# Optimization experiments

Measured on AMD Instinct MI355X. Metric: run time of the kernel, lower is better.

## Reference

```python
import jax, jax.numpy as jnp
import numpy as np

B, DZ, L = 1, 128, 256
H, DC = 4, 32
DHC = H * DC


def setup_inputs() -> dict:
    key = jax.random.key(0)
    ks = jax.random.split(key, 6)
    s = 0.02
    return {
        "z": jax.random.normal(ks[0], (B, DZ, L, L), dtype=jnp.float32),
        "ln_w": jnp.ones((DZ,), jnp.float32),
        "ln_b": jnp.zeros((DZ,), jnp.float32),
        "wq": jax.random.normal(ks[1], (DZ, DHC), jnp.float32) * s,
        "bq": jnp.zeros((DHC,), jnp.float32),
        "wk": jax.random.normal(ks[2], (DZ, DHC), jnp.float32) * s,
        "bk": jnp.zeros((DHC,), jnp.float32),
        "wv": jax.random.normal(ks[3], (DZ, DHC), jnp.float32) * s,
        "bv": jnp.zeros((DHC,), jnp.float32),
        "wg": jax.random.normal(ks[4], (DZ, DHC), jnp.float32) * s,
        "bg": jnp.zeros((DHC,), jnp.float32),
        "w2": jax.random.normal(ks[5], (DHC, DZ), jnp.float32) * s,
        "b2": jnp.zeros((DZ,), jnp.float32),
    }


def reference(z, ln_w, ln_b, wq, bq, wk, bk, wv, bv, wg, bg, w2, b2):
    # z: (B, C, L, L) -> (B, n, i, dz)
    zp = jnp.transpose(z, (0, 2, 3, 1))
    # LayerNorm over last dim (torch eps=1e-5)
    mu = jnp.mean(zp, axis=-1, keepdims=True)
    var = jnp.mean(jnp.square(zp - mu), axis=-1, keepdims=True)
    zn = (zp - mu) * jax.lax.rsqrt(var + 1e-5) * ln_w + ln_b

    def proj(w, b):  # (B,n,i,dz) -> (B,n,i,H,DC)
        return (zn @ w + b).reshape(zn.shape[:-1] + (H, DC))

    scalar = jnp.sqrt(jnp.float32(1.0 / DC))
    q = proj(wq, bq)
    k = proj(wk, bk)
    v = proj(wv, bv)
    attn = jnp.einsum('bnihc,bnjhc->bhnij', q * scalar, k)
    attn_w = jax.nn.softmax(attn, axis=-1)
    o = jnp.einsum('bhnij,bnjhc->bnihc', attn_w, v)
    g = jax.nn.sigmoid(zn @ wg + bg).reshape(o.shape)
    zo = (o * g).reshape(o.shape[:-2] + (DHC,))
    out = (zo @ w2 + b2)
    return jnp.transpose(out, (0, 3, 1, 2))  # (B, C, L, L)
```

## Files before the change

kernel.cpp:

```cpp
#include <hip/hip_runtime.h>
#include <cstdint>
#include <cstddef>

#define DZc   128
#define Lc    256
#define Hc    4
#define DCc   32
#define DHCc  128
#define NPOSc (Lc * Lc)

typedef __attribute__((ext_vector_type(8))) short bf16x8;
typedef __attribute__((ext_vector_type(4))) short bf16x4;
typedef __attribute__((ext_vector_type(4))) float f32x4;

static __device__ __forceinline__ unsigned short f2bf(float f) {
  unsigned u = __float_as_uint(f);
  u += 0x7FFFu + ((u >> 16) & 1u);
  return (unsigned short)(u >> 16);
}
static __device__ __forceinline__ float bf2f(unsigned short h) {
  return __uint_as_float(((unsigned)h) << 16);
}
static __device__ __forceinline__ float sigmoidf_(float x) {
  return 1.0f / (1.0f + __expf(-x));
}
static __device__ __forceinline__ unsigned cvtpk(float lo, float hi) {
  unsigned r;
  asm("v_cvt_pk_bf16_f32 %0, %1, %2" : "=v"(r) : "v"(lo), "v"(hi));
  return r;
}

__global__ __launch_bounds__(256) void prep_weights(
    const float* __restrict__ wq, const float* __restrict__ wk,
    const float* __restrict__ wv, const float* __restrict__ wg,
    const float* __restrict__ w2, unsigned short* __restrict__ wT)
{
  const int b = blockIdx.x;
  const int t = threadIdx.x;
  const float* src = (b == 0) ? wq : (b == 1) ? wk : (b == 2) ? wv : (b == 3) ? wg : w2;
  unsigned short* dst = wT + (size_t)b * (DZc * DHCc);
  const float scale = (b == 0) ? 0.17677669529663687f : 1.0f;
  for (int p = 0; p < 64; ++p) {
    const int idx = p * 256 + t;
    const int kk = idx >> 7, j = idx & 127;
    dst[j * 128 + kk] = f2bf(src[idx] * scale);
  }
}

__global__ __launch_bounds__(512, 2) void fused_ln_proj_attn(
    const float* __restrict__ z, const float* __restrict__ lnw, const float* __restrict__ lnb,
    const unsigned short* __restrict__ wT,
    const float* __restrict__ bq, const float* __restrict__ bk,
    const float* __restrict__ bv, const float* __restrict__ bg,
    unsigned short* __restrict__ og_ws)
{
  __shared__ unsigned short zkl[Lc * DZc];
  __shared__ unsigned short vtl[DHCc * Lc];
  __shared__ unsigned short pll[8][16 * 64];

  const int t  = threadIdx.x;
  const int n  = blockIdx.x;
  const int w8 = t >> 6;
  const int l  = t & 63;
  const int lr = l & 15;
  const int lg = l >> 4;
  const int h     = w8 & 3;
  const int ihalf = w8 >> 2;

  char* zkb = reinterpret_cast<char*>(zkl);
  char* vtb = reinterpret_cast<char*>(vtl);
  char* plb = reinterpret_cast<char*>(&pll[w8][0]);

  #pragma unroll
  for (int p = 0; p < 2; ++p) {
    const int pq = t >> 4;
    const int cg = t & 15;
    const int gp = n * 256 + p * 128 + pq * 4;
    const int cbase = cg * 8;

    float4 zr[8];
    #pragma unroll
    for (int cc = 0; cc < 8; ++cc)
      zr[cc] = *reinterpret_cast<const float4*>(&z[(size_t)(cbase + cc) * NPOSc + gp]);

    float s[4] = {0.f, 0.f, 0.f, 0.f}, s2[4] = {0.f, 0.f, 0.f, 0.f};
    #pragma unroll
    for (int cc = 0; cc < 8; ++cc) {
      s[0] += zr[cc].x; s2[0] += zr[cc].x * zr[cc].x;
      s[1] += zr[cc].y; s2[1] += zr[cc].y * zr[cc].y;
      s[2] += zr[cc].z; s2[2] += zr[cc].z * zr[cc].z;
      s[3] += zr[cc].w; s2[3] += zr[cc].w * zr[cc].w;
    }
    #pragma unroll
    for (int m = 1; m <= 8; m <<= 1) {
      #pragma unroll
      for (int e = 0; e < 4; ++e) {
        s[e]  += __shfl_xor(s[e],  m);
        s2[e] += __shfl_xor(s2[e], m);
      }
    }
    float mu[4], rs[4];
    #pragma unroll
    for (int e = 0; e < 4; ++e) {
      mu[e] = s[e] * (1.0f / DZc);
      const float var = s2[e] * (1.0f / DZc) - mu[e] * mu[e];
      rs[e] = rsqrtf(var + 1e-5f);
    }
    float lw[8], lb[8];
    #pragma unroll
    for (int q4 = 0; q4 < 2; ++q4) {
      const float4 a = *reinterpret_cast<const float4*>(&lnw[cbase + q4 * 4]);
      const float4 b = *reinterpret_cast<const float4*>(&lnb[cbase + q4 * 4]);
      lw[q4 * 4 + 0] = a.x; lw[q4 * 4 + 1] = a.y; lw[q4 * 4 + 2] = a.z; lw[q4 * 4 + 3] = a.w;
      lb[q4 * 4 + 0] = b.x; lb[q4 * 4 + 1] = b.y; lb[q4 * 4 + 2] = b.z; lb[q4 * 4 + 3] = b.w;
    }
    #pragma unroll
    for (int e = 0; e < 4; ++e) {
      const int i = p * 128 + pq * 4 + e;
      float zn[8];
      #pragma unroll
      for (int cc = 0; cc < 8; ++cc) {
        const float zc = (e == 0) ? zr[cc].x : (e == 1) ? zr[cc].y
                       : (e == 2) ? zr[cc].z : zr[cc].w;
        zn[cc] = (zc - mu[e]) * rs[e] * lw[cc] + lb[cc];
      }
      uint4 pw;
      pw.x = cvtpk(zn[0], zn[1]); pw.y = cvtpk(zn[2], zn[3]);
      pw.z = cvtpk(zn[4], zn[5]); pw.w = cvtpk(zn[6], zn[7]);
      int byte = i * 256 + cbase * 2;
      byte ^= ((i & 15) << 4);
      *reinterpret_cast<uint4*>(zkb + byte) = pw;
    }
  }
  __syncthreads();

  const unsigned short* wqT = wT;
  const unsigned short* wkT = wT + 1 * (DZc * DHCc);
  const unsigned short* wvT = wT + 2 * (DZc * DHCc);
  const unsigned short* wgT = wT + 3 * (DZc * DHCc);

  bf16x8 qfrag[8];
  {
    bf16x8 bfq[2][4];
    float4 qb4[2];
    #pragma unroll
    for (int jt = 0; jt < 2; ++jt) {
      #pragma unroll
      for (int kt = 0; kt < 4; ++kt)
        bfq[jt][kt] = *reinterpret_cast<const bf16x8*>(
            &wqT[(size_t)(h * 32 + jt * 16 + lr) * 128 + kt * 32 + lg * 8]);
      qb4[jt] = *reinterpret_cast<const float4*>(&bq[h * 32 + jt * 16 + lg * 4]);
      qb4[jt].x *= 0.17677669529663687f; qb4[jt].y *= 0.17677669529663687f;
      qb4[jt].z *= 0.17677669529663687f; qb4[jt].w *= 0.17677669529663687f;
    }
    #pragma unroll
    for (int it = 0; it < 8; ++it) {
      bf16x8 af[4];
      #pragma unroll
      for (int kt = 0; kt < 4; ++kt) {
        const int i = ihalf * 128 + it * 16 + lr;
        int byte = i * 256 + (kt * 64 + lg * 16);
        byte ^= ((i & 15) << 4);
        af[kt] = *reinterpret_cast<const bf16x8*>(zkb + byte);
      }
      f32x4 qa[2];
      qa[0] = (f32x4){0.f, 0.f, 0.f, 0.f};
      qa[1] = (f32x4){0.f, 0.f, 0.f, 0.f};
      #pragma unroll
      for (int kt = 0; kt < 4; ++kt)
        #pragma unroll
        for (int jt = 0; jt < 2; ++jt)
          qa[jt] = __builtin_amdgcn_mfma_f32_16x16x32_bf16(bfq[jt][kt], af[kt], qa[jt], 0, 0, 0);
      unsigned srcw0[2], srcw1[2];
      srcw0[0] = cvtpk(qa[0][0] + qb4[0].x, qa[0][1] + qb4[0].y);
      srcw0[1] = cvtpk(qa[0][2] + qb4[0].z, qa[0][3] + qb4[0].w);
      srcw1[0] = cvtpk(qa[1][0] + qb4[1].x, qa[1][1] + qb4[1].y);
      srcw1[1] = cvtpk(qa[1][2] + qb4[1].z, qa[1][3] + qb4[1].w);
      unsigned qw[4];
      #pragma unroll
      for (int i4 = 0; i4 < 4; ++i4) {
        const int quad = lg * 2 + (i4 >> 1);
        const int srcl = (quad & 3) * 16 + lr;
        const unsigned a = (unsigned)__shfl((int)srcw0[i4 & 1], srcl);
        const unsigned b = (unsigned)__shfl((int)srcw1[i4 & 1], srcl);
        qw[i4] = (lg >= 2) ? b : a;
      }
      uint4 qv; qv.x = qw[0]; qv.y = qw[1]; qv.z = qw[2]; qv.w = qw[3];
      qfrag[it] = *reinterpret_cast<const bf16x8*>(&qv);
    }
  }

  unsigned gpk[8][2][2];
  {
    bf16x8 bfg[2][4];
    float gb[2];
    #pragma unroll
    for (int jt = 0; jt < 2; ++jt) {
      #pragma unroll
      for (int kt = 0; kt < 4; ++kt)
        bfg[jt][kt] = *reinterpret_cast<const bf16x8*>(
            &wgT[(size_t)(h * 32 + jt * 16 + lr) * 128 + kt * 32 + lg * 8]);
      gb[jt] = bg[h * 32 + jt * 16 + lr];
    }
    #pragma unroll
    for (int it = 0; it < 8; ++it) {
      bf16x8 af[4];
      #pragma unroll
      for (int kt = 0; kt < 4; ++kt) {
        const int i = ihalf * 128 + it * 16 + lr;
        int byte = i * 256 + (kt * 64 + lg * 16);
        byte ^= ((i & 15) << 4);
        af[kt] = *reinterpret_cast<const bf16x8*>(zkb + byte);
      }
      f32x4 ga[2];
      ga[0] = (f32x4){0.f, 0.f, 0.f, 0.f};
      ga[1] = (f32x4){0.f, 0.f, 0.f, 0.f};
      #pragma unroll
      for (int kt = 0; kt < 4; ++kt)
        #pragma unroll
        for (int jt = 0; jt < 2; ++jt)
          ga[jt] = __builtin_amdgcn_mfma_f32_16x16x32_bf16(af[kt], bfg[jt][kt], ga[jt], 0, 0, 0);
      #pragma unroll
      for (int jt = 0; jt < 2; ++jt) {
        gpk[it][jt][0] = cvtpk(sigmoidf_(ga[jt][0] + gb[jt]), sigmoidf_(ga[jt][1] + gb[jt]));
        gpk[it][jt][1] = cvtpk(sigmoidf_(ga[jt][2] + gb[jt]), sigmoidf_(ga[jt][3] + gb[jt]));
      }
    }
  }

  {
    const int chq = w8 & 3, vih = w8 >> 2;
    bf16x8 bfv[2][4];
    float vb[2];
    #pragma unroll
    for (int jt = 0; jt < 2; ++jt) {
      #pragma unroll
      for (int kt = 0; kt < 4; ++kt)
        bfv[jt][kt] = *reinterpret_cast<const bf16x8*>(
            &wvT[(size_t)(chq * 32 + jt * 16 + lr) * 128 + kt * 32 + lg * 8]);
      vb[jt] = bv[chq * 32 + jt * 16 + lr];
    }
    #pragma unroll 1
    for (int it = 0; it < 8; ++it) {
      bf16x8 af[4];
      #pragma unroll
      for (int kt = 0; kt < 4; ++kt) {
        const int i = vih * 128 + it * 16 + lr;
        int byte = i * 256 + (kt * 64 + lg * 16);
        byte ^= ((i & 15) << 4);
        af[kt] = *reinterpret_cast<const bf16x8*>(zkb + byte);
      }
      f32x4 va[2];
      va[0] = (f32x4){0.f, 0.f, 0.f, 0.f};
      va[1] = (f32x4){0.f, 0.f, 0.f, 0.f};
      #pragma unroll
      for (int kt = 0; kt < 4; ++kt)
        #pragma unroll
        for (int jt = 0; jt < 2; ++jt)
          va[jt] = __builtin_amdgcn_mfma_f32_16x16x32_bf16(af[kt], bfv[jt][kt], va[jt], 0, 0, 0);
      const int ii0 = vih * 128 + it * 16 + lg * 4;
      #pragma unroll
      for (int jt = 0; jt < 2; ++jt) {
        const int ch = chq * 32 + jt * 16 + lr;
        uint2 pv;
        pv.x = cvtpk(va[jt][0] + vb[jt], va[jt][1] + vb[jt]);
        pv.y = cvtpk(va[jt][2] + vb[jt], va[jt][3] + vb[jt]);
        int byte = ch * 512 + ii0 * 2;
        byte ^= ((ch & 7) << 4);
        *reinterpret_cast<uint2*>(vtb + byte) = pv;
      }
    }
  }

  {
    bf16x8 bfk[4];
    #pragma unroll
    for (int kt = 0; kt < 4; ++kt)
      bfk[kt] = *reinterpret_cast<const bf16x8*>(
          &wkT[(size_t)(w8 * 16 + lr) * 128 + kt * 32 + lg * 8]);
    const float4 kb4 = *reinterpret_cast<const float4*>(&bk[w8 * 16 + lg * 4]);
    const float kb[4] = {kb4.x, kb4.y, kb4.z, kb4.w};

    #pragma unroll 1
    for (int c = 0; c < 4; ++c) {
      bf16x8 afr[4][4];
      #pragma unroll
      for (int itc = 0; itc < 4; ++itc)
        #pragma unroll
        for (int kt = 0; kt < 4; ++kt) {
          const int i = c * 64 + itc * 16 + lr;
          int byte = i * 256 + (kt * 64 + lg * 16);
          byte ^= ((i & 15) << 4);
          afr[itc][kt] = *reinterpret_cast<const bf16x8*>(zkb + byte);
        }
      __syncthreads();
      #pragma unroll
      for (int itc = 0; itc < 4; ++itc) {
        f32x4 ka = (f32x4){0.f, 0.f, 0.f, 0.f};
        #pragma unroll
        for (int kt = 0; kt < 4; ++kt)
          ka = __builtin_amdgcn_mfma_f32_16x16x32_bf16(bfk[kt], afr[itc][kt], ka, 0, 0, 0);
        const int j = c * 64 + itc * 16 + lr;
        uint2 pkk;
        pkk.x = cvtpk(ka[0] + kb[0], ka[1] + kb[1]);
        pkk.y = cvtpk(ka[2] + kb[2], ka[3] + kb[3]);
        int byte = j * 256 + (w8 * 16 + lg * 4) * 2;
        byte ^= ((j & 15) << 4);
        *reinterpret_cast<uint2*>(zkb + byte) = pkk;
      }
      __syncthreads();
    }
  }

  #pragma unroll
  for (int it = 0; it < 8; ++it) {
    f32x4 sacc[16];
    #pragma unroll
    for (int jt = 0; jt < 16; ++jt) sacc[jt] = (f32x4){0.f, 0.f, 0.f, 0.f};
    #pragma unroll
    for (int jt = 0; jt < 16; ++jt) {
      const int j = jt * 16 + lr;
      int byte = j * 256 + h * 64 + lg * 16;
      byte ^= ((j & 15) << 4);
      bf16x8 kf = *reinterpret_cast<const bf16x8*>(zkb + byte);
      sacc[jt] = __builtin_amdgcn_mfma_f32_16x16x32_bf16(kf, qfrag[it], sacc[jt], 0, 0, 0);
    }

    float psum = 0.f;
    #pragma unroll
    for (int jt = 0; jt < 16; ++jt)
      #pragma unroll
      for (int r = 0; r < 4; ++r) {
        const float e = __expf(sacc[jt][r]);
        sacc[jt][r] = e;
        psum += e;
      }
    psum += __shfl_xor(psum, 16);
    psum += __shfl_xor(psum, 32);
    const float rl = 1.0f / psum;

    f32x4 oacc[2];
    oacc[0] = (f32x4){0.f, 0.f, 0.f, 0.f};
    oacc[1] = (f32x4){0.f, 0.f, 0.f, 0.f};
    #pragma unroll
    for (int qr = 0; qr < 4; ++qr) {
      #pragma unroll
      for (int jj = 0; jj < 4; ++jj) {
        const int jt = qr * 4 + jj;
        uint2 pk;
        pk.x = cvtpk(sacc[jt][0], sacc[jt][1]);
        pk.y = cvtpk(sacc[jt][2], sacc[jt][3]);
        int byte = lr * 128 + (jj * 16 + lg * 4) * 2;
        byte ^= ((lr & 7) << 4);
        *reinterpret_cast<uint2*>(plb + byte) = pk;
      }
      asm volatile("s_waitcnt lgkmcnt(0)" ::: "memory");
      __builtin_amdgcn_sched_barrier(0);
      #pragma unroll
      for (int kq = 0; kq < 2; ++kq) {
        int pbyte = lr * 128 + (kq * 64 + lg * 16);
        pbyte ^= ((lr & 7) << 4);
        bf16x8 pf = *reinterpret_cast<const bf16x8*>(plb + pbyte);
        #pragma unroll
        for (int cht = 0; cht < 2; ++cht) {
          const int ch = h * 32 + cht * 16 + lr;
          int vbyte = ch * 512 + (qr * 128 + kq * 64 + lg * 16);
          vbyte ^= ((ch & 7) << 4);
          bf16x8 vf = *reinterpret_cast<const bf16x8*>(vtb + vbyte);
          oacc[cht] = __builtin_amdgcn_mfma_f32_16x16x32_bf16(pf, vf, oacc[cht], 0, 0, 0);
        }
      }
    }

    #pragma unroll
    for (int cht = 0; cht < 2; ++cht)
      #pragma unroll
      for (int r = 0; r < 4; ++r) {
        const int i = ihalf * 128 + it * 16 + lg * 4 + r;
        const float gv = bf2f((unsigned short)((gpk[it][cht][r >> 1] >> ((r & 1) * 16)) & 0xffff));
        const size_t off = ((size_t)(n * Lc + i)) * 128 + h * 32 + cht * 16 + lr;
        og_ws[off] = f2bf(oacc[cht][r] * rl * gv);
      }
  }
}

__global__ __launch_bounds__(256) void outproj_mfma(
    const unsigned short* __restrict__ og_ws,
    const unsigned short* __restrict__ w2T, const float* __restrict__ b2,
    float* __restrict__ out)
{
  const int t = threadIdx.x;
  const int w = t >> 6, l = t & 63, lr = l & 15, lg = l >> 4;
  const int pos = blockIdx.x * 64 + w * 16 + lr;

  bf16x8 zb[4];
  #pragma unroll
  for (int kt = 0; kt < 4; ++kt)
    zb[kt] = *reinterpret_cast<const bf16x8*>(
        &og_ws[(size_t)pos * 128 + kt * 32 + lg * 8]);

  #pragma unroll
  for (int ct = 0; ct < 8; ++ct) {
    f32x4 acc = (f32x4){0.f, 0.f, 0.f, 0.f};
    #pragma unroll
    for (int kt = 0; kt < 4; ++kt) {
      bf16x8 af = *reinterpret_cast<const bf16x8*>(
          &w2T[(size_t)(ct * 16 + lr) * 128 + kt * 32 + lg * 8]);
      acc = __builtin_amdgcn_mfma_f32_16x16x32_bf16(af, zb[kt], acc, 0, 0, 0);
    }
    #pragma unroll
    for (int r = 0; r < 4; ++r) {
      const int c = ct * 16 + lg * 4 + r;
      out[(size_t)c * NPOSc + pos] = acc[r] + b2[c];
    }
  }
}

extern "C" void kernel_launch(void* const* d_in, const int* in_sizes, int n_in,
                              void* d_out, int out_size, void* d_ws, size_t ws_size,
                              hipStream_t stream) {
  const float* z   = (const float*)d_in[0];
  const float* lnw = (const float*)d_in[1];
  const float* lnb = (const float*)d_in[2];
  const float* wq  = (const float*)d_in[3];
  const float* bq  = (const float*)d_in[4];
  const float* wk  = (const float*)d_in[5];
  const float* bk  = (const float*)d_in[6];
  const float* wv  = (const float*)d_in[7];
  const float* bv  = (const float*)d_in[8];
  const float* wg  = (const float*)d_in[9];
  const float* bg  = (const float*)d_in[10];
  const float* w2  = (const float*)d_in[11];
  const float* b2  = (const float*)d_in[12];
  float* out = (float*)d_out;

  const size_t S = (size_t)NPOSc * DHCc;
  unsigned short* ws = (unsigned short*)d_ws;
  unsigned short* og_ws = ws;
  unsigned short* wT    = ws + S;

  prep_weights<<<5, 256, 0, stream>>>(wq, wk, wv, wg, w2, wT);
  fused_ln_proj_attn<<<Lc, 512, 0, stream>>>(
      z, lnw, lnb, wT, bq, bk, bv, bg, og_ws);
  outproj_mfma<<<NPOSc / 64, 256, 0, stream>>>(
      og_ws, wT + 4 * (DZc * DHCc), b2, out);
}
```

Before: 80.07 us.

## Use 1024-thread blocks with 16 waves splitting rows into quarters

Doubles the fused attention block from 8 to 16 wavefronts. Each wave now handles a quarter of the query rows per head instead of a half, and the LN, Q/G/V/K projection loops are re-split to match. The goal is more parallel waves per row-block, hiding latency and cutting per-wave serial work. In exchange, each CU holds one large block instead of two, shared memory grows for the extra P buffers, and the per-thread register budget tightens.

```diff
diff --git a/kernel.cpp b/kernel.cpp
--- a/kernel.cpp
+++ b/kernel.cpp
@@ -47,7 +47,7 @@
   }
 }
 
-__global__ __launch_bounds__(512, 2) void fused_ln_proj_attn(
+__global__ __launch_bounds__(1024) void fused_ln_proj_attn(
     const float* __restrict__ z, const float* __restrict__ lnw, const float* __restrict__ lnb,
     const unsigned short* __restrict__ wT,
     const float* __restrict__ bq, const float* __restrict__ bk,
@@ -56,26 +56,25 @@
 {
   __shared__ unsigned short zkl[Lc * DZc];
   __shared__ unsigned short vtl[DHCc * Lc];
-  __shared__ unsigned short pll[8][16 * 64];
+  __shared__ unsigned short pll[16][16 * 64];
 
   const int t  = threadIdx.x;
   const int n  = blockIdx.x;
-  const int w8 = t >> 6;
+  const int w16 = t >> 6;
   const int l  = t & 63;
   const int lr = l & 15;
   const int lg = l >> 4;
-  const int h     = w8 & 3;
-  const int ihalf = w8 >> 2;
+  const int h  = w16 & 3;
+  const int iq = w16 >> 2;
 
   char* zkb = reinterpret_cast<char*>(zkl);
   char* vtb = reinterpret_cast<char*>(vtl);
-  char* plb = reinterpret_cast<char*>(&pll[w8][0]);
-
-  #pragma unroll
-  for (int p = 0; p < 2; ++p) {
+  char* plb = reinterpret_cast<char*>(&pll[w16][0]);
+
+  {
     const int pq = t >> 4;
     const int cg = t & 15;
-    const int gp = n * 256 + p * 128 + pq * 4;
+    const int gp = n * 256 + pq * 4;
     const int cbase = cg * 8;
 
     float4 zr[8];
@@ -116,7 +115,7 @@
     }
     #pragma unroll
     for (int e = 0; e < 4; ++e) {
-      const int i = p * 128 + pq * 4 + e;
+      const int i = pq * 4 + e;
       float zn[8];
       #pragma unroll
       for (int cc = 0; cc < 8; ++cc) {
@@ -139,7 +138,7 @@
   const unsigned short* wvT = wT + 2 * (DZc * DHCc);
   const unsigned short* wgT = wT + 3 * (DZc * DHCc);
 
-  bf16x8 qfrag[8];
+  bf16x8 qfrag[4];
   {
     bf16x8 bfq[2][4];
     float4 qb4[2];
@@ -154,11 +153,11 @@
       qb4[jt].z *= 0.17677669529663687f; qb4[jt].w *= 0.17677669529663687f;
     }
     #pragma unroll
-    for (int it = 0; it < 8; ++it) {
+    for (int it = 0; it < 4; ++it) {
       bf16x8 af[4];
       #pragma unroll
       for (int kt = 0; kt < 4; ++kt) {
-        const int i = ihalf * 128 + it * 16 + lr;
+        const int i = iq * 64 + it * 16 + lr;
         int byte = i * 256 + (kt * 64 + lg * 16);
         byte ^= ((i & 15) << 4);
         af[kt] = *reinterpret_cast<const bf16x8*>(zkb + byte);
@@ -190,7 +189,7 @@
     }
   }
 
-  unsigned gpk[8][2][2];
+  unsigned gpk[4][2][2];
   {
     bf16x8 bfg[2][4];
     float gb[2];
@@ -203,11 +202,11 @@
       gb[jt] = bg[h * 32 + jt * 16 + lr];
     }
     #pragma unroll
-    for (int it = 0; it < 8; ++it) {
+    for (int it = 0; it < 4; ++it) {
       bf16x8 af[4];
       #pragma unroll
       for (int kt = 0; kt < 4; ++kt) {
-        const int i = ihalf * 128 + it * 16 + lr;
+        const int i = iq * 64 + it * 16 + lr;
         int byte = i * 256 + (kt * 64 + lg * 16);
         byte ^= ((i & 15) << 4);
         af[kt] = *reinterpret_cast<const bf16x8*>(zkb + byte);
@@ -229,7 +228,7 @@
   }
 
   {
-    const int chq = w8 & 3, vih = w8 >> 2;
+    const int chq = w16 & 3, vq = w16 >> 2;
     bf16x8 bfv[2][4];
     float vb[2];
     #pragma unroll
@@ -241,11 +240,11 @@
       vb[jt] = bv[chq * 32 + jt * 16 + lr];
     }
     #pragma unroll 1
-    for (int it = 0; it < 8; ++it) {
+    for (int it = 0; it < 4; ++it) {
       bf16x8 af[4];
       #pragma unroll
       for (int kt = 0; kt < 4; ++kt) {
-        const int i = vih * 128 + it * 16 + lr;
+        const int i = vq * 64 + it * 16 + lr;
         int byte = i * 256 + (kt * 64 + lg * 16);
         byte ^= ((i & 15) << 4);
         af[kt] = *reinterpret_cast<const bf16x8*>(zkb + byte);
@@ -258,7 +257,7 @@
         #pragma unroll
         for (int jt = 0; jt < 2; ++jt)
           va[jt] = __builtin_amdgcn_mfma_f32_16x16x32_bf16(af[kt], bfv[jt][kt], va[jt], 0, 0, 0);
-      const int ii0 = vih * 128 + it * 16 + lg * 4;
+      const int ii0 = vq * 64 + it * 16 + lg * 4;
       #pragma unroll
       for (int jt = 0; jt < 2; ++jt) {
         const int ch = chq * 32 + jt * 16 + lr;
@@ -273,22 +272,23 @@
   }
 
   {
+    const int cho = w16 & 7, rh = w16 >> 3;
     bf16x8 bfk[4];
     #pragma unroll
     for (int kt = 0; kt < 4; ++kt)
       bfk[kt] = *reinterpret_cast<const bf16x8*>(
-          &wkT[(size_t)(w8 * 16 + lr) * 128 + kt * 32 + lg * 8]);
-    const float4 kb4 = *reinterpret_cast<const float4*>(&bk[w8 * 16 + lg * 4]);
+          &wkT[(size_t)(cho * 16 + lr) * 128 + kt * 32 + lg * 8]);
+    const float4 kb4 = *reinterpret_cast<const float4*>(&bk[cho * 16 + lg * 4]);
     const float kb[4] = {kb4.x, kb4.y, kb4.z, kb4.w};
 
     #pragma unroll 1
-    for (int c = 0; c < 4; ++c) {
+    for (int c = 0; c < 2; ++c) {
       bf16x8 afr[4][4];
       #pragma unroll
       for (int itc = 0; itc < 4; ++itc)
         #pragma unroll
         for (int kt = 0; kt < 4; ++kt) {
-          const int i = c * 64 + itc * 16 + lr;
+          const int i = rh * 128 + c * 64 + itc * 16 + lr;
           int byte = i * 256 + (kt * 64 + lg * 16);
           byte ^= ((i & 15) << 4);
           afr[itc][kt] = *reinterpret_cast<const bf16x8*>(zkb + byte);
@@ -300,11 +300,11 @@
         #pragma unroll
         for (int kt = 0; kt < 4; ++kt)
           ka = __builtin_amdgcn_mfma_f32_16x16x32_bf16(bfk[kt], afr[itc][kt], ka, 0, 0, 0);
-        const int j = c * 64 + itc * 16 + lr;
+        const int j = rh * 128 + c * 64 + itc * 16 + lr;
         uint2 pkk;
         pkk.x = cvtpk(ka[0] + kb[0], ka[1] + kb[1]);
         pkk.y = cvtpk(ka[2] + kb[2], ka[3] + kb[3]);
-        int byte = j * 256 + (w8 * 16 + lg * 4) * 2;
+        int byte = j * 256 + (cho * 16 + lg * 4) * 2;
         byte ^= ((j & 15) << 4);
         *reinterpret_cast<uint2*>(zkb + byte) = pkk;
       }
@@ -313,7 +313,7 @@
   }
 
   #pragma unroll
-  for (int it = 0; it < 8; ++it) {
+  for (int it = 0; it < 4; ++it) {
     f32x4 sacc[16];
     #pragma unroll
     for (int jt = 0; jt < 16; ++jt) sacc[jt] = (f32x4){0.f, 0.f, 0.f, 0.f};
@@ -376,7 +376,7 @@
     for (int cht = 0; cht < 2; ++cht)
       #pragma unroll
       for (int r = 0; r < 4; ++r) {
-        const int i = ihalf * 128 + it * 16 + lg * 4 + r;
+        const int i = iq * 64 + it * 16 + lg * 4 + r;
         const float gv = bf2f((unsigned short)((gpk[it][cht][r >> 1] >> ((r & 1) * 16)) & 0xffff));
         const size_t off = ((size_t)(n * Lc + i)) * 128 + h * 32 + cht * 16 + lr;
         og_ws[off] = f2bf(oacc[cht][r] * rl * gv);
@@ -440,7 +440,7 @@
   unsigned short* wT    = ws + S;
 
   prep_weights<<<5, 256, 0, stream>>>(wq, wk, wv, wg, w2, wT);
-  fused_ln_proj_attn<<<Lc, 512, 0, stream>>>(
+  fused_ln_proj_attn<<<Lc, 1024, 0, stream>>>(
       z, lnw, lnb, wT, bq, bk, bv, bg, og_ws);
   outproj_mfma<<<NPOSc / 64, 256, 0, stream>>>(
       og_ws, wT + 4 * (DZc * DHCc), b2, out);
```

Result: slower. 87.07 us (+8.7%).

## Fuse output projection into attention kernel epilogue

Applied to the files above, without the earlier changes.

Removes the separate outproj kernel launch and performs the W2 projection at the end of the fused attention kernel. Each block waits for its own gated-output writes to global memory, synchronizes, then reads them back (likely from L2) and computes the output projection for its row of 256 positions. This saves a kernel launch and lets the og workspace reads hit cache, but the epilogue runs on only 256 blocks and lengthens the main kernel's tail.

```diff
diff --git a/kernel.cpp b/kernel.cpp
--- a/kernel.cpp
+++ b/kernel.cpp
@@ -52,7 +52,8 @@
     const unsigned short* __restrict__ wT,
     const float* __restrict__ bq, const float* __restrict__ bk,
     const float* __restrict__ bv, const float* __restrict__ bg,
-    unsigned short* __restrict__ og_ws)
+    const float* __restrict__ b2,
+    unsigned short* __restrict__ og_ws, float* __restrict__ out)
 {
   __shared__ unsigned short zkl[Lc * DZc];
   __shared__ unsigned short vtl[DHCc * Lc];
@@ -382,36 +383,40 @@
         og_ws[off] = f2bf(oacc[cht][r] * rl * gv);
       }
   }
-}
-
-__global__ __launch_bounds__(256) void outproj_mfma(
-    const unsigned short* __restrict__ og_ws,
-    const unsigned short* __restrict__ w2T, const float* __restrict__ b2,
-    float* __restrict__ out)
-{
-  const int t = threadIdx.x;
-  const int w = t >> 6, l = t & 63, lr = l & 15, lg = l >> 4;
-  const int pos = blockIdx.x * 64 + w * 16 + lr;
-
-  bf16x8 zb[4];
-  #pragma unroll
-  for (int kt = 0; kt < 4; ++kt)
-    zb[kt] = *reinterpret_cast<const bf16x8*>(
-        &og_ws[(size_t)pos * 128 + kt * 32 + lg * 8]);
-
-  #pragma unroll
-  for (int ct = 0; ct < 8; ++ct) {
-    f32x4 acc = (f32x4){0.f, 0.f, 0.f, 0.f};
-    #pragma unroll
-    for (int kt = 0; kt < 4; ++kt) {
-      bf16x8 af = *reinterpret_cast<const bf16x8*>(
-          &w2T[(size_t)(ct * 16 + lr) * 128 + kt * 32 + lg * 8]);
-      acc = __builtin_amdgcn_mfma_f32_16x16x32_bf16(af, zb[kt], acc, 0, 0, 0);
-    }
-    #pragma unroll
-    for (int r = 0; r < 4; ++r) {
-      const int c = ct * 16 + lg * 4 + r;
-      out[(size_t)c * NPOSc + pos] = acc[r] + b2[c];
+
+  asm volatile("s_waitcnt vmcnt(0)" ::: "memory");
+  __syncthreads();
+  {
+    const unsigned short* w2T = wT + 4 * (DZc * DHCc);
+    bf16x8 zb[2][4];
+    #pragma unroll
+    for (int sub = 0; sub < 2; ++sub) {
+      const size_t gpos = (size_t)n * 256 + w8 * 32 + sub * 16 + lr;
+      #pragma unroll
+      for (int kt = 0; kt < 4; ++kt)
+        zb[sub][kt] = *reinterpret_cast<const bf16x8*>(
+            &og_ws[gpos * 128 + kt * 32 + lg * 8]);
+    }
+    #pragma unroll
+    for (int ct = 0; ct < 8; ++ct) {
+      bf16x8 af[4];
+      #pragma unroll
+      for (int kt = 0; kt < 4; ++kt)
+        af[kt] = *reinterpret_cast<const bf16x8*>(
+            &w2T[(size_t)(ct * 16 + lr) * 128 + kt * 32 + lg * 8]);
+      #pragma unroll
+      for (int sub = 0; sub < 2; ++sub) {
+        f32x4 acc = (f32x4){0.f, 0.f, 0.f, 0.f};
+        #pragma unroll
+        for (int kt = 0; kt < 4; ++kt)
+          acc = __builtin_amdgcn_mfma_f32_16x16x32_bf16(af[kt], zb[sub][kt], acc, 0, 0, 0);
+        const size_t gpos = (size_t)n * 256 + w8 * 32 + sub * 16 + lr;
+        #pragma unroll
+        for (int r = 0; r < 4; ++r) {
+          const int c = ct * 16 + lg * 4 + r;
+          out[(size_t)c * NPOSc + gpos] = acc[r] + b2[c];
+        }
+      }
     }
   }
 }
@@ -441,7 +446,5 @@
 
   prep_weights<<<5, 256, 0, stream>>>(wq, wk, wv, wg, w2, wT);
   fused_ln_proj_attn<<<Lc, 512, 0, stream>>>(
-      z, lnw, lnb, wT, bq, bk, bv, bg, og_ws);
-  outproj_mfma<<<NPOSc / 64, 256, 0, stream>>>(
-      og_ws, wT + 4 * (DZc * DHCc), b2, out);
-}
+      z, lnw, lnb, wT, bq, bk, bv, bg, b2, og_ws, out);
+}
```

Result: faster. 69.84 us (-12.8%).
